# Performance work log

Measured on AMD Instinct MI355X. Metric: run time of the kernel, lower is better.

## Reference

```python
import jax, jax.numpy as jnp
import numpy as np

N, F_IN, F_OUT, HEADS = 4096, 128, 64, 4


def setup_inputs() -> dict:
    key = jax.random.key(0)
    k1, k2, k3, k4, k5 = jax.random.split(key, 5)
    X = jax.random.normal(k1, (N, F_IN), dtype=jnp.float32)
    A = jax.random.randint(k2, (N, N), 0, 2, dtype=jnp.int32)
    # zero the diagonal: the torch loop always prepends the self node, so the
    # adjacency must not also contain it (would duplicate the self term).
    A = A * (1 - jnp.eye(N, dtype=jnp.int32))
    # per-head Linear(F_IN, F_OUT) weights/bias and Linear(2*F_OUT, 1, bias=False)
    W = jax.random.normal(k3, (HEADS, F_OUT, F_IN), dtype=jnp.float32) / np.sqrt(F_IN)
    b = jax.random.normal(k4, (HEADS, F_OUT), dtype=jnp.float32) * 0.02
    att = jax.random.normal(k5, (HEADS, 2 * F_OUT), dtype=jnp.float32) / np.sqrt(2 * F_OUT)
    return {"X": X, "A": A, "W": W, "b": b, "att": att}


def reference(X, A, W, b, att):
    # H[h, n, o] = line_h(X)
    H = jnp.einsum('nf,hof->hno', X, W) + b[:, None, :]
    f_out = W.shape[1]
    a_src, a_dst = att[:, :f_out], att[:, f_out:]
    # score e_ij = leaky_relu(a_src.H_i + a_dst.H_j)
    s = jnp.einsum('hno,ho->hn', H, a_src)  # query-side term (xi_bar expanded)
    d = jnp.einsum('hno,ho->hn', H, a_dst)  # neighbor-side term
    e = jax.nn.leaky_relu(s[:, :, None] + d[:, None, :])  # [H, N, N]
    # neighbor set = {self} U {j : A_ij != 0}
    mask = (A > 0) | jnp.eye(A.shape[0], dtype=bool)
    e = jnp.where(mask[None], e, -jnp.inf)
    alpha = jax.nn.softmax(e, axis=-1)  # segment softmax per node row
    # weighted sum per head, then mean over heads (sum / head in the original)
    out = jnp.einsum('hnm,hmo->no', alpha, H) / W.shape[0]
    return out  # [N, F_OUT]
```

## Files before the change

kernel.cpp:

```cpp
#include <hip/hip_runtime.h>
#include <hip/hip_bf16.h>


#define NN 4096
#define FIN 128
#define FOUT 64
#define NH 4

typedef __attribute__((ext_vector_type(8))) short bf16x8;
typedef __attribute__((ext_vector_type(4))) float f32x4;
typedef __attribute__((ext_vector_type(4))) unsigned int u32x4;

__device__ __forceinline__ unsigned short f32_bf16(float f) {
    unsigned u = __builtin_bit_cast(unsigned, f);
    u += 0x7fffu + ((u >> 16) & 1u);
    return (unsigned short)(u >> 16);
}

__device__ __forceinline__ void gload16(const void* g, void* l) {
    __builtin_amdgcn_global_load_lds(
        (const __attribute__((address_space(1))) unsigned*)g,
        (__attribute__((address_space(3))) unsigned*)l, 16, 0, 0);
}

__global__ __launch_bounds__(256) void pack_bits(
    const int* __restrict__ A, unsigned long long* __restrict__ Abits)
{
    const int row  = blockIdx.x;
    const int lane = threadIdx.x & 63;
    const int wv   = threadIdx.x >> 6;
    const int* arow = A + (size_t)row * NN;
    #pragma unroll 4
    for (int c = 0; c < 16; ++c) {
        const int col = c * 256 + wv * 64 + lane;
        unsigned long long m = __ballot(__builtin_nontemporal_load(&arow[col]) > 0);
        if (lane == 0) Abits[(size_t)row * 64 + c * 4 + wv] = m;
    }
}

__global__ __launch_bounds__(256) void gat_prep(
    const float* __restrict__ X, const float* __restrict__ W,
    const float* __restrict__ b, const float* __restrict__ att,
    unsigned short* __restrict__ HbfT, float* __restrict__ Hrow,
    float* __restrict__ s_out, float* __restrict__ d_out,
    float* __restrict__ es_g, float* __restrict__ es2_g,
    float* __restrict__ ed_g, float* __restrict__ ed2_g)
{
    const int rb = blockIdx.x;
    const int h  = blockIdx.y;
    const int n0 = rb * 32;
    const int t  = threadIdx.x;

    __shared__ float Xl[32][132];
    __shared__ float Wt[128][68];

    for (int g = t; g < 32 * 32; g += 256) {
        int row = g >> 5, c4 = g & 31;
        float4 v = *(const float4*)&X[(size_t)(n0 + row) * FIN + c4 * 4];
        *(float4*)&Xl[row][c4 * 4] = v;
    }
    for (int g = t; g < 64 * 32; g += 256) {
        int o = g >> 5, c4 = g & 31;
        float4 v = *(const float4*)&W[((size_t)h * FOUT + o) * FIN + c4 * 4];
        Wt[c4 * 4 + 0][o] = v.x; Wt[c4 * 4 + 1][o] = v.y;
        Wt[c4 * 4 + 2][o] = v.z; Wt[c4 * 4 + 3][o] = v.w;
    }
    __syncthreads();

    const int rg = t >> 4;
    const int og = t & 15;
    float acc[2][4] = {};

    #pragma unroll 4
    for (int f4 = 0; f4 < 32; ++f4) {
        float xv[2][4], wv[4][4];
        #pragma unroll
        for (int i = 0; i < 2; ++i) {
            float4 tmp = *(const float4*)&Xl[rg * 2 + i][f4 * 4];
            xv[i][0] = tmp.x; xv[i][1] = tmp.y; xv[i][2] = tmp.z; xv[i][3] = tmp.w;
        }
        #pragma unroll
        for (int k = 0; k < 4; ++k) {
            float4 tmp = *(const float4*)&Wt[f4 * 4 + k][og * 4];
            wv[k][0] = tmp.x; wv[k][1] = tmp.y; wv[k][2] = tmp.z; wv[k][3] = tmp.w;
        }
        #pragma unroll
        for (int i = 0; i < 2; ++i)
            #pragma unroll
            for (int k = 0; k < 4; ++k)
                #pragma unroll
                for (int jj = 0; jj < 4; ++jj)
                    acc[i][jj] = fmaf(xv[i][k], wv[k][jj], acc[i][jj]);
    }

    float bb[4], as_[4], ad_[4];
    #pragma unroll
    for (int jj = 0; jj < 4; ++jj) {
        bb[jj]  = b[h * FOUT + og * 4 + jj];
        as_[jj] = att[h * 2 * FOUT + og * 4 + jj];
        ad_[jj] = att[h * 2 * FOUT + FOUT + og * 4 + jj];
    }
    #pragma unroll
    for (int i = 0; i < 2; ++i)
        #pragma unroll
        for (int jj = 0; jj < 4; ++jj)
            acc[i][jj] += bb[jj];

    float sp[2] = {0.f, 0.f}, dp[2] = {0.f, 0.f};
    #pragma unroll
    for (int i = 0; i < 2; ++i)
        #pragma unroll
        for (int jj = 0; jj < 4; ++jj) {
            sp[i] = fmaf(acc[i][jj], as_[jj], sp[i]);
            dp[i] = fmaf(acc[i][jj], ad_[jj], dp[i]);
        }
    #pragma unroll
    for (int off = 1; off < 16; off <<= 1) {
        #pragma unroll
        for (int i = 0; i < 2; ++i) {
            sp[i] += __shfl_xor(sp[i], off);
            dp[i] += __shfl_xor(dp[i], off);
        }
    }
    if (og == 0) {
        #pragma unroll
        for (int i = 0; i < 2; ++i) {
            int nn = n0 + rg * 2 + i;
            s_out[h * NN + nn]  = sp[i];
            d_out[h * NN + nn]  = dp[i];
            es_g [h * NN + nn]  = __expf(sp[i]);
            es2_g[h * NN + nn]  = __expf(0.01f * sp[i]);
            ed_g [h * NN + nn]  = __expf(dp[i]);
            ed2_g[h * NN + nn]  = __expf(0.01f * dp[i]);
        }
    }

    #pragma unroll
    for (int i = 0; i < 2; ++i) {
        float4 v = make_float4(acc[i][0], acc[i][1], acc[i][2], acc[i][3]);
        *(float4*)&Hrow[((size_t)h * NN + n0 + rg * 2 + i) * FOUT + og * 4] = v;
    }
    #pragma unroll
    for (int jj = 0; jj < 4; ++jj) {
        int o = og * 4 + jj;
        ushort2 p;
        p.x = f32_bf16(acc[0][jj]);
        p.y = f32_bf16(acc[1][jj]);
        *(ushort2*)&HbfT[((size_t)h * FOUT + o) * NN + n0 + rg * 2] = p;
    }
}

struct SMem {
    union {
        __align__(16) unsigned short H[2][64][256];
        struct {
            float red[6][16][68];
            float redl[6][16];
        } fin;
    };
    unsigned bits[2][32][8];
    float ed [2][256];
    float ed2[2][256];
};

__global__ __launch_bounds__(512, 4) void gat_main(
    const unsigned* __restrict__ Abits, const unsigned short* __restrict__ HbfT,
    const float* __restrict__ s_g, const float* __restrict__ d_g,
    const float* __restrict__ es_g, const float* __restrict__ es2_g,
    const float* __restrict__ ed_g, const float* __restrict__ ed2_g,
    const float* __restrict__ Hrow, float* __restrict__ outH)
{
    const int id   = blockIdx.x;
    const int h    = id & 3;
    const int tile = id >> 2;
    const int n0   = tile * 32;
    const int tid  = threadIdx.x;
    const int w    = tid >> 6;
    const int lane = tid & 63;
    const int r    = lane & 15;
    const int q    = lane >> 4;
    const int qs   = q * 8;
    const int rg   = w & 1;
    const int kg   = w >> 1;

    __shared__ SMem sm;

    const int nrow = n0 + rg * 16 + r;
    const float es  = es_g [h * NN + nrow];
    const float es2 = es2_g[h * NN + nrow];

    const int bb = ((kg * 4 + q) ^ r) & 15;

    const int blk = lane & 31;
    const unsigned short* gH[4];
    #pragma unroll
    for (int i = 0; i < 4; ++i) {
        const int row = 8 * w + 2 * i + (lane >> 5);
        const int gb  = ((blk & 15) ^ (row & 15)) | (blk & 16);
        gH[i] = HbfT + ((size_t)(h * FOUT) + row) * NN + gb * 8;
    }
    const unsigned* gBits = Abits + (size_t)(n0 + (lane >> 1)) * 128 + (lane & 1) * 4;
    const float* gEd  = ed_g  + (size_t)h * NN + lane * 4;
    const float* gEd2 = ed2_g + (size_t)h * NN + lane * 4;

    bf16x8 ones;
    #pragma unroll
    for (int i = 0; i < 8; ++i) ones[i] = (short)0x3F80;

    f32x4 acc0 = {0,0,0,0}, acc1 = {0,0,0,0}, acc2 = {0,0,0,0},
          acc3 = {0,0,0,0}, accl = {0,0,0,0};

    {
        unsigned short* hw = &sm.H[0][8 * w][0];
        gload16(gH[0], hw);
        gload16(gH[1], hw +  512);
        gload16(gH[2], hw + 1024);
        gload16(gH[3], hw + 1536);
        if      (w == 0) gload16(gBits, &sm.bits[0][0][0]);
        else if (w == 1) gload16(gEd,   &sm.ed [0][0]);
        else if (w == 2) gload16(gEd2,  &sm.ed2[0][0]);
    }
    __syncthreads();

    #pragma unroll 2
    for (int ch = 0; ch < 16; ++ch) {
        const int buf = ch & 1;

        if (ch < 15) {
            const int nb   = buf ^ 1;
            const int coff = (ch + 1) * 256;
            unsigned short* hw = &sm.H[nb][8 * w][0];
            gload16(gH[0] + coff, hw);
            gload16(gH[1] + coff, hw +  512);
            gload16(gH[2] + coff, hw + 1024);
            gload16(gH[3] + coff, hw + 1536);
            if      (w == 0) gload16(gBits + (ch + 1) * 8, &sm.bits[nb][0][0]);
            else if (w == 1) gload16(gEd  + coff, &sm.ed [nb][0]);
            else if (w == 2) gload16(gEd2 + coff, &sm.ed2[nb][0]);
        }

        {
            const unsigned bits8 = sm.bits[buf][rg * 16 + r][kg] >> qs;
            const float4 e0 = *(const float4*)&sm.ed [buf][kg * 32 + qs];
            const float4 e1 = *(const float4*)&sm.ed [buf][kg * 32 + qs + 4];
            const float4 g0 = *(const float4*)&sm.ed2[buf][kg * 32 + qs];
            const float4 g1 = *(const float4*)&sm.ed2[buf][kg * 32 + qs + 4];
            const float edv [8] = {e0.x, e0.y, e0.z, e0.w, e1.x, e1.y, e1.z, e1.w};
            const float ed2v[8] = {g0.x, g0.y, g0.z, g0.w, g1.x, g1.y, g1.z, g1.w};
            u32x4 afu;
            #pragma unroll
            for (int p = 0; p < 4; ++p) {
                const int j0 = 2 * p, j1 = 2 * p + 1;
                float wa = (bits8 & (1u << j0))
                         ? fmaxf(es * edv[j0], es2 * ed2v[j0]) : 0.0f;
                float wb = (bits8 & (1u << j1))
                         ? fmaxf(es * edv[j1], es2 * ed2v[j1]) : 0.0f;
                __hip_bfloat162 pk = __float22bfloat162_rn(make_float2(wa, wb));
                unsigned u;
                __builtin_memcpy(&u, &pk, sizeof(u));
                afu[p] = u;
            }
            const bf16x8 af = __builtin_bit_cast(bf16x8, afu);

            const bf16x8 b0 = *(const bf16x8*)&sm.H[buf][r     ][bb * 8];
            const bf16x8 b1 = *(const bf16x8*)&sm.H[buf][r + 16][bb * 8];
            const bf16x8 b2 = *(const bf16x8*)&sm.H[buf][r + 32][bb * 8];
            const bf16x8 b3 = *(const bf16x8*)&sm.H[buf][r + 48][bb * 8];

            acc0 = __builtin_amdgcn_mfma_f32_16x16x32_bf16(af, b0,   acc0, 0, 0, 0);
            acc1 = __builtin_amdgcn_mfma_f32_16x16x32_bf16(af, b1,   acc1, 0, 0, 0);
            acc2 = __builtin_amdgcn_mfma_f32_16x16x32_bf16(af, b2,   acc2, 0, 0, 0);
            acc3 = __builtin_amdgcn_mfma_f32_16x16x32_bf16(af, b3,   acc3, 0, 0, 0);
            accl = __builtin_amdgcn_mfma_f32_16x16x32_bf16(af, ones, accl, 0, 0, 0);
        }

        {
            const unsigned bits8 = sm.bits[buf][rg * 16 + r][kg + 4] >> qs;
            const float4 e0 = *(const float4*)&sm.ed [buf][128 + kg * 32 + qs];
            const float4 e1 = *(const float4*)&sm.ed [buf][128 + kg * 32 + qs + 4];
            const float4 g0 = *(const float4*)&sm.ed2[buf][128 + kg * 32 + qs];
            const float4 g1 = *(const float4*)&sm.ed2[buf][128 + kg * 32 + qs + 4];
            const float edv [8] = {e0.x, e0.y, e0.z, e0.w, e1.x, e1.y, e1.z, e1.w};
            const float ed2v[8] = {g0.x, g0.y, g0.z, g0.w, g1.x, g1.y, g1.z, g1.w};
            u32x4 afu;
            #pragma unroll
            for (int p = 0; p < 4; ++p) {
                const int j0 = 2 * p, j1 = 2 * p + 1;
                float wa = (bits8 & (1u << j0))
                         ? fmaxf(es * edv[j0], es2 * ed2v[j0]) : 0.0f;
                float wb = (bits8 & (1u << j1))
                         ? fmaxf(es * edv[j1], es2 * ed2v[j1]) : 0.0f;
                __hip_bfloat162 pk = __float22bfloat162_rn(make_float2(wa, wb));
                unsigned u;
                __builtin_memcpy(&u, &pk, sizeof(u));
                afu[p] = u;
            }
            const bf16x8 af = __builtin_bit_cast(bf16x8, afu);

            const bf16x8 b0 = *(const bf16x8*)&sm.H[buf][r     ][128 + bb * 8];
            const bf16x8 b1 = *(const bf16x8*)&sm.H[buf][r + 16][128 + bb * 8];
            const bf16x8 b2 = *(const bf16x8*)&sm.H[buf][r + 32][128 + bb * 8];
            const bf16x8 b3 = *(const bf16x8*)&sm.H[buf][r + 48][128 + bb * 8];

            acc0 = __builtin_amdgcn_mfma_f32_16x16x32_bf16(af, b0,   acc0, 0, 0, 0);
            acc1 = __builtin_amdgcn_mfma_f32_16x16x32_bf16(af, b1,   acc1, 0, 0, 0);
            acc2 = __builtin_amdgcn_mfma_f32_16x16x32_bf16(af, b2,   acc2, 0, 0, 0);
            acc3 = __builtin_amdgcn_mfma_f32_16x16x32_bf16(af, b3,   acc3, 0, 0, 0);
            accl = __builtin_amdgcn_mfma_f32_16x16x32_bf16(af, ones, accl, 0, 0, 0);
        }

        __syncthreads();
    }

    if (kg > 0) {
        const int widx = (kg - 1) * 2 + rg;
        #pragma unroll
        for (int reg = 0; reg < 4; ++reg) {
            const int rr = q * 4 + reg;
            sm.fin.red[widx][rr][ 0 + r] = acc0[reg];
            sm.fin.red[widx][rr][16 + r] = acc1[reg];
            sm.fin.red[widx][rr][32 + r] = acc2[reg];
            sm.fin.red[widx][rr][48 + r] = acc3[reg];
        }
        if (r == 0) {
            #pragma unroll
            for (int reg = 0; reg < 4; ++reg)
                sm.fin.redl[widx][q * 4 + reg] = accl[reg];
        }
    }
    __syncthreads();
    if (kg == 0) {
        #pragma unroll
        for (int kk = 0; kk < 3; ++kk) {
            const int widx = kk * 2 + rg;
            #pragma unroll
            for (int reg = 0; reg < 4; ++reg) {
                const int rr = q * 4 + reg;
                acc0[reg] += sm.fin.red[widx][rr][ 0 + r];
                acc1[reg] += sm.fin.red[widx][rr][16 + r];
                acc2[reg] += sm.fin.red[widx][rr][32 + r];
                acc3[reg] += sm.fin.red[widx][rr][48 + r];
                accl[reg] += sm.fin.redl[widx][rr];
            }
        }
        #pragma unroll
        for (int reg = 0; reg < 4; ++reg) {
            const int rr  = q * 4 + reg;
            const int nn2 = n0 + rg * 16 + rr;
            const float tt = s_g[h * NN + nn2] + d_g[h * NN + nn2];
            const float wd = __expf(fmaxf(tt, 0.01f * tt));
            const float inv = 0.25f / (accl[reg] + wd);
            const float* hr = &Hrow[((size_t)h * NN + nn2) * FOUT];
            float*       ob = &outH[((size_t)h * NN + nn2) * FOUT];
            ob[ 0 + r] = (acc0[reg] + wd * hr[ 0 + r]) * inv;
            ob[16 + r] = (acc1[reg] + wd * hr[16 + r]) * inv;
            ob[32 + r] = (acc2[reg] + wd * hr[32 + r]) * inv;
            ob[48 + r] = (acc3[reg] + wd * hr[48 + r]) * inv;
        }
    }
}

__global__ __launch_bounds__(256) void gat_fin(
    const float* __restrict__ outH, float* __restrict__ out)
{
    const int i = blockIdx.x * 256 + threadIdx.x;
    const f32x4* p = (const f32x4*)outH;
    f32x4 v0 = __builtin_nontemporal_load(p + i);
    f32x4 v1 = __builtin_nontemporal_load(p + i +  65536);
    f32x4 v2 = __builtin_nontemporal_load(p + i + 131072);
    f32x4 v3 = __builtin_nontemporal_load(p + i + 196608);
    f32x4 s = (v0 + v1) + (v2 + v3);
    *((f32x4*)out + i) = s;
}

extern "C" void kernel_launch(void* const* d_in, const int* in_sizes, int n_in,
                              void* d_out, int out_size, void* d_ws, size_t ws_size,
                              hipStream_t stream) {
    const float* X   = (const float*)d_in[0];
    const int*   A   = (const int*)  d_in[1];
    const float* W   = (const float*)d_in[2];
    const float* b   = (const float*)d_in[3];
    const float* att = (const float*)d_in[4];
    float* out = (float*)d_out;

    char* ws = (char*)d_ws;
    unsigned short* HbfT = (unsigned short*)ws;
    size_t off = (size_t)NH * FOUT * NN * 2;
    float* s_buf   = (float*)(ws + off);  off += (size_t)NH * NN * 4;
    float* d_buf   = (float*)(ws + off);  off += (size_t)NH * NN * 4;
    float* es_buf  = (float*)(ws + off);  off += (size_t)NH * NN * 4;
    float* es2_buf = (float*)(ws + off);  off += (size_t)NH * NN * 4;
    float* ed_buf  = (float*)(ws + off);  off += (size_t)NH * NN * 4;
    float* ed2_buf = (float*)(ws + off);  off += (size_t)NH * NN * 4;
    unsigned long long* Abits = (unsigned long long*)(ws + off);
    off += (size_t)NN * 64 * 8;
    float* Hrow   = (float*)(ws + off);
    off += (size_t)NH * NN * FOUT * 4;
    float* outH   = (float*)(ws + off);
    off += (size_t)NH * NN * FOUT * 4;

    pack_bits<<<NN, 256, 0, stream>>>(A, Abits);
    gat_prep<<<dim3(128, 4), 256, 0, stream>>>(X, W, b, att, HbfT, Hrow,
                                               s_buf, d_buf,
                                               es_buf, es2_buf, ed_buf, ed2_buf);
    gat_main<<<512, 512, 0, stream>>>((const unsigned*)Abits, HbfT,
                                      s_buf, d_buf,
                                      es_buf, es2_buf, ed_buf, ed2_buf,
                                      Hrow, outH);
    gat_fin<<<256, 256, 0, stream>>>(outH, out);
}
```

Before: 157.6 us.

## Remap waves so each covers both row groups for one k slice

Changes the wave-to-work mapping in the main GAT kernel. Each of the 8 waves now handles one 32-column k slice for both 16-row groups instead of two k slices for one row group. Each H fragment read from shared memory is reused across two A fragments, which halves the LDS traffic for H. In exchange, accumulator register use doubles and the final cross-wave reduction grows from 6 to 7 partial sets of 32 rows each, costing more shared memory and reduction work.

```diff
diff --git a/kernel.cpp b/kernel.cpp
--- a/kernel.cpp
+++ b/kernel.cpp
@@ -154,8 +154,8 @@
     union {
         __align__(16) unsigned short H[2][64][256];
         struct {
-            float red[6][16][68];
-            float redl[6][16];
+            float red[7][32][68];
+            float redl[7][32];
         } fin;
     };
     unsigned bits[2][32][8];
@@ -180,16 +180,16 @@
     const int r    = lane & 15;
     const int q    = lane >> 4;
     const int qs   = q * 8;
-    const int rg   = w & 1;
-    const int kg   = w >> 1;
 
     __shared__ SMem sm;
 
-    const int nrow = n0 + rg * 16 + r;
-    const float es  = es_g [h * NN + nrow];
-    const float es2 = es2_g[h * NN + nrow];
-
-    const int bb = ((kg * 4 + q) ^ r) & 15;
+    const float es_a  = es_g [h * NN + n0 + r];
+    const float es2_a = es2_g[h * NN + n0 + r];
+    const float es_b  = es_g [h * NN + n0 + 16 + r];
+    const float es2_b = es2_g[h * NN + n0 + 16 + r];
+
+    const int cb   = w * 4 + q;
+    const int sblk = ((cb & 15) ^ r) | (cb & 16);
 
     const int blk = lane & 31;
     const unsigned short* gH[4];
@@ -207,8 +207,10 @@
     #pragma unroll
     for (int i = 0; i < 8; ++i) ones[i] = (short)0x3F80;
 
-    f32x4 acc0 = {0,0,0,0}, acc1 = {0,0,0,0}, acc2 = {0,0,0,0},
-          acc3 = {0,0,0,0}, accl = {0,0,0,0};
+    f32x4 a0 = {0,0,0,0}, a1 = {0,0,0,0}, a2 = {0,0,0,0},
+          a3 = {0,0,0,0}, al = {0,0,0,0};
+    f32x4 b0a = {0,0,0,0}, b1a = {0,0,0,0}, b2a = {0,0,0,0},
+          b3a = {0,0,0,0}, bla = {0,0,0,0};
 
     {
         unsigned short* hw = &sm.H[0][8 * w][0];
@@ -239,123 +241,124 @@
             else if (w == 2) gload16(gEd2 + coff, &sm.ed2[nb][0]);
         }
 
-        {
-            const unsigned bits8 = sm.bits[buf][rg * 16 + r][kg] >> qs;
-            const float4 e0 = *(const float4*)&sm.ed [buf][kg * 32 + qs];
-            const float4 e1 = *(const float4*)&sm.ed [buf][kg * 32 + qs + 4];
-            const float4 g0 = *(const float4*)&sm.ed2[buf][kg * 32 + qs];
-            const float4 g1 = *(const float4*)&sm.ed2[buf][kg * 32 + qs + 4];
-            const float edv [8] = {e0.x, e0.y, e0.z, e0.w, e1.x, e1.y, e1.z, e1.w};
-            const float ed2v[8] = {g0.x, g0.y, g0.z, g0.w, g1.x, g1.y, g1.z, g1.w};
-            u32x4 afu;
-            #pragma unroll
-            for (int p = 0; p < 4; ++p) {
-                const int j0 = 2 * p, j1 = 2 * p + 1;
-                float wa = (bits8 & (1u << j0))
-                         ? fmaxf(es * edv[j0], es2 * ed2v[j0]) : 0.0f;
-                float wb = (bits8 & (1u << j1))
-                         ? fmaxf(es * edv[j1], es2 * ed2v[j1]) : 0.0f;
-                __hip_bfloat162 pk = __float22bfloat162_rn(make_float2(wa, wb));
-                unsigned u;
-                __builtin_memcpy(&u, &pk, sizeof(u));
-                afu[p] = u;
-            }
-            const bf16x8 af = __builtin_bit_cast(bf16x8, afu);
-
-            const bf16x8 b0 = *(const bf16x8*)&sm.H[buf][r     ][bb * 8];
-            const bf16x8 b1 = *(const bf16x8*)&sm.H[buf][r + 16][bb * 8];
-            const bf16x8 b2 = *(const bf16x8*)&sm.H[buf][r + 32][bb * 8];
-            const bf16x8 b3 = *(const bf16x8*)&sm.H[buf][r + 48][bb * 8];
-
-            acc0 = __builtin_amdgcn_mfma_f32_16x16x32_bf16(af, b0,   acc0, 0, 0, 0);
-            acc1 = __builtin_amdgcn_mfma_f32_16x16x32_bf16(af, b1,   acc1, 0, 0, 0);
-            acc2 = __builtin_amdgcn_mfma_f32_16x16x32_bf16(af, b2,   acc2, 0, 0, 0);
-            acc3 = __builtin_amdgcn_mfma_f32_16x16x32_bf16(af, b3,   acc3, 0, 0, 0);
-            accl = __builtin_amdgcn_mfma_f32_16x16x32_bf16(af, ones, accl, 0, 0, 0);
-        }
-
-        {
-            const unsigned bits8 = sm.bits[buf][rg * 16 + r][kg + 4] >> qs;
-            const float4 e0 = *(const float4*)&sm.ed [buf][128 + kg * 32 + qs];
-            const float4 e1 = *(const float4*)&sm.ed [buf][128 + kg * 32 + qs + 4];
-            const float4 g0 = *(const float4*)&sm.ed2[buf][128 + kg * 32 + qs];
-            const float4 g1 = *(const float4*)&sm.ed2[buf][128 + kg * 32 + qs + 4];
-            const float edv [8] = {e0.x, e0.y, e0.z, e0.w, e1.x, e1.y, e1.z, e1.w};
-            const float ed2v[8] = {g0.x, g0.y, g0.z, g0.w, g1.x, g1.y, g1.z, g1.w};
-            u32x4 afu;
-            #pragma unroll
-            for (int p = 0; p < 4; ++p) {
-                const int j0 = 2 * p, j1 = 2 * p + 1;
-                float wa = (bits8 & (1u << j0))
-                         ? fmaxf(es * edv[j0], es2 * ed2v[j0]) : 0.0f;
-                float wb = (bits8 & (1u << j1))
-                         ? fmaxf(es * edv[j1], es2 * ed2v[j1]) : 0.0f;
-                __hip_bfloat162 pk = __float22bfloat162_rn(make_float2(wa, wb));
-                unsigned u;
-                __builtin_memcpy(&u, &pk, sizeof(u));
-                afu[p] = u;
-            }
-            const bf16x8 af = __builtin_bit_cast(bf16x8, afu);
-
-            const bf16x8 b0 = *(const bf16x8*)&sm.H[buf][r     ][128 + bb * 8];
-            const bf16x8 b1 = *(const bf16x8*)&sm.H[buf][r + 16][128 + bb * 8];
-            const bf16x8 b2 = *(const bf16x8*)&sm.H[buf][r + 32][128 + bb * 8];
-            const bf16x8 b3 = *(const bf16x8*)&sm.H[buf][r + 48][128 + bb * 8];
-
-            acc0 = __builtin_amdgcn_mfma_f32_16x16x32_bf16(af, b0,   acc0, 0, 0, 0);
-            acc1 = __builtin_amdgcn_mfma_f32_16x16x32_bf16(af, b1,   acc1, 0, 0, 0);
-            acc2 = __builtin_amdgcn_mfma_f32_16x16x32_bf16(af, b2,   acc2, 0, 0, 0);
-            acc3 = __builtin_amdgcn_mfma_f32_16x16x32_bf16(af, b3,   acc3, 0, 0, 0);
-            accl = __builtin_amdgcn_mfma_f32_16x16x32_bf16(af, ones, accl, 0, 0, 0);
-        }
+        const float4 e0 = *(const float4*)&sm.ed [buf][w * 32 + qs];
+        const float4 e1 = *(const float4*)&sm.ed [buf][w * 32 + qs + 4];
+        const float4 g0 = *(const float4*)&sm.ed2[buf][w * 32 + qs];
+        const float4 g1 = *(const float4*)&sm.ed2[buf][w * 32 + qs + 4];
+        const float edv [8] = {e0.x, e0.y, e0.z, e0.w, e1.x, e1.y, e1.z, e1.w};
+        const float ed2v[8] = {g0.x, g0.y, g0.z, g0.w, g1.x, g1.y, g1.z, g1.w};
+        const unsigned bits8a = sm.bits[buf][r     ][w] >> qs;
+        const unsigned bits8b = sm.bits[buf][r + 16][w] >> qs;
+
+        const bf16x8 f0 = *(const bf16x8*)&sm.H[buf][r     ][sblk * 8];
+        const bf16x8 f1 = *(const bf16x8*)&sm.H[buf][r + 16][sblk * 8];
+        const bf16x8 f2 = *(const bf16x8*)&sm.H[buf][r + 32][sblk * 8];
+        const bf16x8 f3 = *(const bf16x8*)&sm.H[buf][r + 48][sblk * 8];
+
+        u32x4 afuA, afuB;
+        #pragma unroll
+        for (int p = 0; p < 4; ++p) {
+            const int j0 = 2 * p, j1 = 2 * p + 1;
+            float wa = (bits8a & (1u << j0))
+                     ? fmaxf(es_a * edv[j0], es2_a * ed2v[j0]) : 0.0f;
+            float wb = (bits8a & (1u << j1))
+                     ? fmaxf(es_a * edv[j1], es2_a * ed2v[j1]) : 0.0f;
+            __hip_bfloat162 pk = __float22bfloat162_rn(make_float2(wa, wb));
+            unsigned u;
+            __builtin_memcpy(&u, &pk, sizeof(u));
+            afuA[p] = u;
+            float wc = (bits8b & (1u << j0))
+                     ? fmaxf(es_b * edv[j0], es2_b * ed2v[j0]) : 0.0f;
+            float wd = (bits8b & (1u << j1))
+                     ? fmaxf(es_b * edv[j1], es2_b * ed2v[j1]) : 0.0f;
+            __hip_bfloat162 pk2 = __float22bfloat162_rn(make_float2(wc, wd));
+            __builtin_memcpy(&u, &pk2, sizeof(u));
+            afuB[p] = u;
+        }
+        const bf16x8 afA = __builtin_bit_cast(bf16x8, afuA);
+        const bf16x8 afB = __builtin_bit_cast(bf16x8, afuB);
+
+        a0  = __builtin_amdgcn_mfma_f32_16x16x32_bf16(afA, f0,   a0,  0, 0, 0);
+        a1  = __builtin_amdgcn_mfma_f32_16x16x32_bf16(afA, f1,   a1,  0, 0, 0);
+        a2  = __builtin_amdgcn_mfma_f32_16x16x32_bf16(afA, f2,   a2,  0, 0, 0);
+        a3  = __builtin_amdgcn_mfma_f32_16x16x32_bf16(afA, f3,   a3,  0, 0, 0);
+        al  = __builtin_amdgcn_mfma_f32_16x16x32_bf16(afA, ones, al,  0, 0, 0);
+        b0a = __builtin_amdgcn_mfma_f32_16x16x32_bf16(afB, f0,   b0a, 0, 0, 0);
+        b1a = __builtin_amdgcn_mfma_f32_16x16x32_bf16(afB, f1,   b1a, 0, 0, 0);
+        b2a = __builtin_amdgcn_mfma_f32_16x16x32_bf16(afB, f2,   b2a, 0, 0, 0);
+        b3a = __builtin_amdgcn_mfma_f32_16x16x32_bf16(afB, f3,   b3a, 0, 0, 0);
+        bla = __builtin_amdgcn_mfma_f32_16x16x32_bf16(afB, ones, bla, 0, 0, 0);
 
         __syncthreads();
     }
 
-    if (kg > 0) {
-        const int widx = (kg - 1) * 2 + rg;
+    if (w > 0) {
         #pragma unroll
         for (int reg = 0; reg < 4; ++reg) {
             const int rr = q * 4 + reg;
-            sm.fin.red[widx][rr][ 0 + r] = acc0[reg];
-            sm.fin.red[widx][rr][16 + r] = acc1[reg];
-            sm.fin.red[widx][rr][32 + r] = acc2[reg];
-            sm.fin.red[widx][rr][48 + r] = acc3[reg];
+            sm.fin.red[w - 1][rr][ 0 + r] = a0[reg];
+            sm.fin.red[w - 1][rr][16 + r] = a1[reg];
+            sm.fin.red[w - 1][rr][32 + r] = a2[reg];
+            sm.fin.red[w - 1][rr][48 + r] = a3[reg];
+            sm.fin.red[w - 1][16 + rr][ 0 + r] = b0a[reg];
+            sm.fin.red[w - 1][16 + rr][16 + r] = b1a[reg];
+            sm.fin.red[w - 1][16 + rr][32 + r] = b2a[reg];
+            sm.fin.red[w - 1][16 + rr][48 + r] = b3a[reg];
         }
         if (r == 0) {
             #pragma unroll
-            for (int reg = 0; reg < 4; ++reg)
-                sm.fin.redl[widx][q * 4 + reg] = accl[reg];
+            for (int reg = 0; reg < 4; ++reg) {
+                sm.fin.redl[w - 1][q * 4 + reg]      = al[reg];
+                sm.fin.redl[w - 1][16 + q * 4 + reg] = bla[reg];
+            }
         }
     }
     __syncthreads();
-    if (kg == 0) {
-        #pragma unroll
-        for (int kk = 0; kk < 3; ++kk) {
-            const int widx = kk * 2 + rg;
+    if (w == 0) {
+        #pragma unroll
+        for (int kk = 0; kk < 7; ++kk) {
             #pragma unroll
             for (int reg = 0; reg < 4; ++reg) {
                 const int rr = q * 4 + reg;
-                acc0[reg] += sm.fin.red[widx][rr][ 0 + r];
-                acc1[reg] += sm.fin.red[widx][rr][16 + r];
-                acc2[reg] += sm.fin.red[widx][rr][32 + r];
-                acc3[reg] += sm.fin.red[widx][rr][48 + r];
-                accl[reg] += sm.fin.redl[widx][rr];
+                a0[reg]  += sm.fin.red[kk][rr][ 0 + r];
+                a1[reg]  += sm.fin.red[kk][rr][16 + r];
+                a2[reg]  += sm.fin.red[kk][rr][32 + r];
+                a3[reg]  += sm.fin.red[kk][rr][48 + r];
+                al[reg]  += sm.fin.redl[kk][rr];
+                b0a[reg] += sm.fin.red[kk][16 + rr][ 0 + r];
+                b1a[reg] += sm.fin.red[kk][16 + rr][16 + r];
+                b2a[reg] += sm.fin.red[kk][16 + rr][32 + r];
+                b3a[reg] += sm.fin.red[kk][16 + rr][48 + r];
+                bla[reg] += sm.fin.redl[kk][16 + rr];
             }
         }
         #pragma unroll
         for (int reg = 0; reg < 4; ++reg) {
-            const int rr  = q * 4 + reg;
-            const int nn2 = n0 + rg * 16 + rr;
-            const float tt = s_g[h * NN + nn2] + d_g[h * NN + nn2];
-            const float wd = __expf(fmaxf(tt, 0.01f * tt));
-            const float inv = 0.25f / (accl[reg] + wd);
-            const float* hr = &Hrow[((size_t)h * NN + nn2) * FOUT];
-            float*       ob = &outH[((size_t)h * NN + nn2) * FOUT];
-            ob[ 0 + r] = (acc0[reg] + wd * hr[ 0 + r]) * inv;
-            ob[16 + r] = (acc1[reg] + wd * hr[16 + r]) * inv;
-            ob[32 + r] = (acc2[reg] + wd * hr[32 + r]) * inv;
-            ob[48 + r] = (acc3[reg] + wd * hr[48 + r]) * inv;
+            const int rr = q * 4 + reg;
+            {
+                const int nn2 = n0 + rr;
+                const float tt = s_g[h * NN + nn2] + d_g[h * NN + nn2];
+                const float wd = __expf(fmaxf(tt, 0.01f * tt));
+                const float inv = 0.25f / (al[reg] + wd);
+                const float* hr = &Hrow[((size_t)h * NN + nn2) * FOUT];
+                float*       ob = &outH[((size_t)h * NN + nn2) * FOUT];
+                ob[ 0 + r] = (a0[reg] + wd * hr[ 0 + r]) * inv;
+                ob[16 + r] = (a1[reg] + wd * hr[16 + r]) * inv;
+                ob[32 + r] = (a2[reg] + wd * hr[32 + r]) * inv;
+                ob[48 + r] = (a3[reg] + wd * hr[48 + r]) * inv;
+            }
+            {
+                const int nn2 = n0 + 16 + rr;
+                const float tt = s_g[h * NN + nn2] + d_g[h * NN + nn2];
+                const float wd = __expf(fmaxf(tt, 0.01f * tt));
+                const float inv = 0.25f / (bla[reg] + wd);
+                const float* hr = &Hrow[((size_t)h * NN + nn2) * FOUT];
+                float*       ob = &outH[((size_t)h * NN + nn2) * FOUT];
+                ob[ 0 + r] = (b0a[reg] + wd * hr[ 0 + r]) * inv;
+                ob[16 + r] = (b1a[reg] + wd * hr[16 + r]) * inv;
+                ob[32 + r] = (b2a[reg] + wd * hr[32 + r]) * inv;
+                ob[48 + r] = (b3a[reg] + wd * hr[48 + r]) * inv;
+            }
         }
     }
 }
```

After: 158.8 us. Within noise of the previous version (+0.7%).
